# Kernel tuning notes

Measured on AMD Instinct MI355X. Metric: run time of the kernel, lower is better.

## Reference

```python
import jax, jax.numpy as jnp
import numpy as np

N = 50000
E = 800000
F_IN = 64
HID = 64
NCLS = 16


def setup_inputs() -> dict:
    key = jax.random.key(0)
    ks = jax.random.split(key, 8)
    x = jax.random.normal(ks[0], (N, F_IN), dtype=jnp.float32)
    edge_index = jax.random.randint(ks[1], (2, E), 0, N, dtype=jnp.int64)
    edge_weight = jax.random.uniform(ks[2], (E,), dtype=jnp.float32)
    # GCNConv glorot-style weights (PyG stores weight as [in, out]) and zero bias
    W1 = jax.random.normal(ks[3], (F_IN, HID), dtype=jnp.float32) * (1.0 / np.sqrt(F_IN))
    b1 = jnp.zeros((HID,), dtype=jnp.float32)
    W2 = jax.random.normal(ks[4], (HID, HID), dtype=jnp.float32) * (1.0 / np.sqrt(HID))
    b2 = jnp.zeros((HID,), dtype=jnp.float32)
    Wout = jax.random.normal(ks[5], (HID, NCLS), dtype=jnp.float32) * (1.0 / np.sqrt(HID))
    bout = jnp.zeros((NCLS,), dtype=jnp.float32)
    return {"x": x, "edge_index": edge_index, "edge_weight": edge_weight,
            "W1": W1, "b1": b1, "W2": W2, "b2": b2, "Wout": Wout, "bout": bout}


def _gcn_norm(edge_index, edge_weight, num_nodes):
    # PyG gcn_norm with add_self_loops=True (self-loop weight = 1.0)
    row = jnp.concatenate([edge_index[0], jnp.arange(num_nodes, dtype=edge_index.dtype)])
    col = jnp.concatenate([edge_index[1], jnp.arange(num_nodes, dtype=edge_index.dtype)])
    w = jnp.concatenate([edge_weight, jnp.ones((num_nodes,), dtype=edge_weight.dtype)])
    deg = jax.ops.segment_sum(w, col, num_segments=num_nodes)  # [N]
    dinv = jnp.where(deg > 0, jax.lax.rsqrt(deg), 0.0)
    norm = dinv[row] * w * dinv[col]  # [E+N]
    return row, col, norm


def _gcn_conv(h, row, col, norm, W, b, num_nodes):
    h = h @ W                                   # [N, out]
    msg = h[row] * norm[:, None]                # gather + scale, [E+N, out]
    out = jax.ops.segment_sum(msg, col, num_segments=num_nodes)  # scatter-add
    return out + b


def reference(x, edge_index, edge_weight, W1, b1, W2, b2, Wout, bout):
    num_nodes = x.shape[0]
    row, col, norm = _gcn_norm(edge_index, edge_weight, num_nodes)
    h = _gcn_conv(x, row, col, norm, W1, b1, num_nodes)
    h = jax.nn.relu(h)  # dropout is identity in eval mode
    h = _gcn_conv(h, row, col, norm, W2, b2, num_nodes)
    h = jax.nn.relu(h)
    logits = h @ Wout + bout
    return jax.nn.softmax(logits, axis=1)
```

## Files before the change

kernel.cpp:

```cpp
#include <hip/hip_runtime.h>
#include <hip/hip_fp16.h>
#include <math.h>

#define NN 50000
#define NE 800000
#define F 64
#define NCLS 16

#define BKS 7
#define BKN 128
#define NBK 391
#define CAP 2560
#define B1C 4096
#define B1B 196

typedef unsigned short u16;
typedef unsigned int u32;
typedef __attribute__((ext_vector_type(8))) unsigned short ushort8v;

__device__ __forceinline__ float bf2f(u16 h) {
    return __uint_as_float((unsigned)h << 16);
}
__device__ __forceinline__ u16 f2bf(float f) {
    unsigned u = __float_as_uint(f);
    return (u16)((u + 0x7fffu + ((u >> 16) & 1u)) >> 16);
}


__global__ __launch_bounds__(512) void k_local(const int* __restrict__ row,
                                               const int* __restrict__ col,
                                               const float* __restrict__ w,
                                               int2* __restrict__ tmp,
                                               int* __restrict__ ghL,
                                               int* __restrict__ ghH) {
    __shared__ int hist[512], sa[512], sb[512], lcur[512];
    __shared__ int2 stage[B1C];
    int t = threadIdx.x;
    int e0 = blockIdx.x * B1C;
    int cnt = min(B1C, NE - e0);
    hist[t] = 0;
    __syncthreads();

    int mykey[8]; int myb[8]; int myw[8]; bool myv[8];
#pragma unroll
    for (int k = 0; k < 8; ++k) {
        int i = t + k * 512;
        myv[k] = (i < cnt);
        if (myv[k]) {
            int e = e0 + i;
            int c = col[e];
            myb[k]   = c >> BKS;
            mykey[k] = (row[e] << BKS) | (c & (BKN - 1));
            myw[k]   = __float_as_int(w[e]);
            atomicAdd(&hist[myb[k]], 1);
        }
    }
    __syncthreads();

    sa[t] = hist[t];
    __syncthreads();
    int* src = sa; int* dst = sb;
#pragma unroll
    for (int off = 1; off < 512; off <<= 1) {
        dst[t] = src[t] + ((t >= off) ? src[t - off] : 0);
        __syncthreads();
        int* tq = src; src = dst; dst = tq;
    }
    int lex = src[t] - hist[t];
    lcur[t] = lex;
    ghL[blockIdx.x * 512 + t] = lex;
    ghH[blockIdx.x * 512 + t] = hist[t];
    __syncthreads();

#pragma unroll
    for (int k = 0; k < 8; ++k) {
        if (myv[k]) {
            int pos = atomicAdd(&lcur[myb[k]], 1);
            stage[pos] = make_int2(mykey[k], myw[k]);
        }
    }
    __syncthreads();

    for (int i = t; i < cnt; i += 512) tmp[e0 + i] = stage[i];
}


__global__ __launch_bounds__(256) void k_bucket2(const int2* __restrict__ tmp,
                                                 const int* __restrict__ ghL,
                                                 const int* __restrict__ ghH,
                                                 u32* __restrict__ sedge,
                                                 int2* __restrict__ benode,
                                                 float* __restrict__ dinv) {
    __shared__ int2 stage[CAP];
    __shared__ u32 sortedU[CAP];
    __shared__ int lb[200], ps[200];
    __shared__ int ssa[256], ssb[256];
    __shared__ int hist[BKN], na[BKN], nb[BKN], lcur[BKN];
    __shared__ float dsum[BKN];
    int b = blockIdx.x;
    int t = threadIdx.x;
    int lnv = 0;
    if (t < B1B) {
        lb[t] = ghL[t * 512 + b];
        lnv   = ghH[t * 512 + b];
    }
    if (t < BKN) { hist[t] = 0; dsum[t] = 0.f; }
    ssa[t] = lnv;
    __syncthreads();
    int* src = ssa; int* dst = ssb;
#pragma unroll
    for (int off = 1; off < 256; off <<= 1) {
        dst[t] = src[t] + ((t >= off) ? src[t - off] : 0);
        __syncthreads();
        int* tq = src; src = dst; dst = tq;
    }
    if (t < B1B) ps[t] = src[t] - lnv;
    __shared__ int cntS;
    if (t == 0) cntS = src[255];
    __syncthreads();
    int cnt = min(cntS, CAP);

    for (int i = t; i < cnt; i += 256) {
        int lo = 0, hi = B1B;
        while (hi - lo > 1) {
            int mid = (lo + hi) >> 1;
            if (ps[mid] <= i) lo = mid; else hi = mid;
        }
        int2 ed = tmp[lo * B1C + lb[lo] + (i - ps[lo])];
        stage[i] = ed;
        atomicAdd(&hist[ed.x & (BKN - 1)], 1);
        atomicAdd(&dsum[ed.x & (BKN - 1)], __int_as_float(ed.y));
    }
    __syncthreads();
    if (t < BKN) na[t] = hist[t];
    __syncthreads();
    int* s2 = na; int* d2 = nb;
#pragma unroll
    for (int off = 1; off < BKN; off <<= 1) {
        if (t < BKN) d2[t] = s2[t] + ((t >= off) ? s2[t - off] : 0);
        __syncthreads();
        int* tq = s2; s2 = d2; d2 = tq;
    }
    int node0 = b * BKN;
    if (t < BKN) {
        int lincl = s2[t];
        int lexcl = lincl - hist[t];
        lcur[t] = lexcl;
        int node = node0 + t;
        if (node < NN) {
            benode[node] = make_int2(b * CAP + lexcl, b * CAP + lincl);
            dinv[node]   = rsqrtf(1.0f + dsum[t]);
        }
    }
    __syncthreads();
    for (int i = t; i < cnt; i += 256) {
        int2 ed = stage[i];
        int pos = atomicAdd(&lcur[ed.x & (BKN - 1)], 1);
        __half hw = __float2half(__int_as_float(ed.y));
        u32 hb = (u32)__half_as_ushort(hw);
        sortedU[pos] = (hb << 16) | (u32)(ed.x >> BKS);
    }
    __syncthreads();
    for (int i = t; i < cnt; i += 256) sedge[b * CAP + i] = sortedU[i];
}


template<bool BF>
__global__ __launch_bounds__(256) void k_mm64(const void* __restrict__ Xv,
                                              const float* __restrict__ W,
                                              u16* __restrict__ Y) {
    __shared__ float sW[64 * 64];
    __shared__ float sX[16][64];
    int tid = threadIdx.x;
    int c  = tid & 63;
    int wv = tid >> 6;
    for (int i = tid; i < 64 * 64; i += 256) sW[i] = W[i];
    int r0 = blockIdx.x * 16;
#pragma unroll
    for (int i = tid; i < 16 * 64; i += 256) {
        size_t idx = (size_t)(r0 + (i >> 6)) * 64 + (i & 63);
        if (BF) sX[i >> 6][i & 63] = bf2f(((const u16*)Xv)[idx]);
        else    sX[i >> 6][i & 63] = ((const float*)Xv)[idx];
    }
    __syncthreads();
    int rb = wv * 4;
    float a0 = 0.f, a1 = 0.f, a2 = 0.f, a3 = 0.f;
#pragma unroll
    for (int k = 0; k < 64; k += 4) {
        float4 x0 = *(const float4*)&sX[rb + 0][k];
        float4 x1 = *(const float4*)&sX[rb + 1][k];
        float4 x2 = *(const float4*)&sX[rb + 2][k];
        float4 x3 = *(const float4*)&sX[rb + 3][k];
        float wA = sW[(k + 0) * 64 + c];
        float wB = sW[(k + 1) * 64 + c];
        float wC = sW[(k + 2) * 64 + c];
        float wD = sW[(k + 3) * 64 + c];
        a0 += x0.x * wA + x0.y * wB + x0.z * wC + x0.w * wD;
        a1 += x1.x * wA + x1.y * wB + x1.z * wC + x1.w * wD;
        a2 += x2.x * wA + x2.y * wB + x2.z * wC + x2.w * wD;
        a3 += x3.x * wA + x3.y * wB + x3.z * wC + x3.w * wD;
    }
    Y[(size_t)(r0 + rb + 0) * 64 + c] = f2bf(a0);
    Y[(size_t)(r0 + rb + 1) * 64 + c] = f2bf(a1);
    Y[(size_t)(r0 + rb + 2) * 64 + c] = f2bf(a2);
    Y[(size_t)(r0 + rb + 3) * 64 + c] = f2bf(a3);
}


template<bool HEAD>
__global__ __launch_bounds__(256) void k_agg(const u16* __restrict__ A,
                                             const int2* __restrict__ benode,
                                             const u32* __restrict__ sedge,
                                             const float* __restrict__ dinv,
                                             const float* __restrict__ bias,
                                             u16* __restrict__ B,
                                             const float* __restrict__ Wout,
                                             const float* __restrict__ bout,
                                             float* __restrict__ out) {
    __shared__ float sWout[64 * NCLS];
    __shared__ float sh[8][64];
    int tid  = threadIdx.x;
    int wv   = tid >> 6;
    int lane = tid & 63;
    int half = lane >> 5;
    int sub  = lane & 31;
    int slot = sub >> 3;
    int fg   = sub & 7;
    int node = blockIdx.x * 8 + wv * 2 + half;
    if (HEAD) {
        for (int i = tid; i < 64 * NCLS; i += 256) sWout[i] = Wout[i];
    }
    int2 be = benode[node];
    int beg = be.x;
    int deg = be.y - be.x;
    float acc[8] = {0.f, 0.f, 0.f, 0.f, 0.f, 0.f, 0.f, 0.f};

    {
        u32 e = (sub < deg) ? sedge[beg + sub] : 0u;
        int s_own = (int)(e & 0xffffu);
        float wf = __half2float(__ushort_as_half((u16)(e >> 16)));
        float nmr = wf * dinv[s_own];
        int mval = min(32, deg);
#pragma unroll
        for (int t = 0; t < 8; ++t) {
            if ((t << 2) < mval) {
                int idx = (half << 5) + (t << 2) + slot;
                int   s  = __shfl(s_own, idx);
                float nm = __shfl(nmr, idx);
                const ushort8v a = *(const ushort8v*)(A + (size_t)s * 64 + (fg << 3));
#pragma unroll
                for (int j = 0; j < 8; ++j) acc[j] += bf2f(a[j]) * nm;
            }
        }
    }
    for (int base = 32; base < deg; base += 32) {
        int i = base + sub;
        u32 e = (i < deg) ? sedge[beg + i] : 0u;
        int s_own = (int)(e & 0xffffu);
        float wf = __half2float(__ushort_as_half((u16)(e >> 16)));
        float nmr = wf * dinv[s_own];
        int m = min(32, deg - base);
        int steps = (m + 3) >> 2;
        for (int t = 0; t < steps; ++t) {
            int idx = (half << 5) + (t << 2) + slot;
            int   s  = __shfl(s_own, idx);
            float nm = __shfl(nmr, idx);
            const ushort8v a = *(const ushort8v*)(A + (size_t)s * 64 + (fg << 3));
#pragma unroll
            for (int j = 0; j < 8; ++j) acc[j] += bf2f(a[j]) * nm;
        }
    }
#pragma unroll
    for (int o = 8; o <= 16; o <<= 1) {
#pragma unroll
        for (int j = 0; j < 8; ++j) acc[j] += __shfl_xor(acc[j], o);
    }
    if (slot == 0) {
        float d = dinv[node];
        float d2 = d * d;
        const ushort8v self = *(const ushort8v*)(A + (size_t)node * 64 + (fg << 3));
        const float4 bb0 = *(const float4*)(bias + (fg << 3));
        const float4 bb1 = *(const float4*)(bias + (fg << 3) + 4);
        float bbv[8] = {bb0.x, bb0.y, bb0.z, bb0.w, bb1.x, bb1.y, bb1.z, bb1.w};
        ushort8v ov;
#pragma unroll
        for (int j = 0; j < 8; ++j) {
            float v = fmaxf(acc[j] * d + bf2f(self[j]) * d2 + bbv[j], 0.f);
            ov[j] = f2bf(v);
            if (HEAD) sh[wv * 2 + half][(fg << 3) + j] = v;
        }
        *(ushort8v*)(B + (size_t)node * 64 + (fg << 3)) = ov;
    }
    if (HEAD) {
        __syncthreads();
        int nib  = tid >> 5;
        int sub2 = tid & 31;
        int c = sub2 & 15, q = sub2 >> 4;
        const float* hrow = sh[nib];
        float p = 0.f;
#pragma unroll
        for (int k = 0; k < 32; ++k)
            p += hrow[q * 32 + k] * sWout[(q * 32 + k) * NCLS + c];
        p += __shfl_xor(p, 16);
        p += bout[c];
        float mx = p;
#pragma unroll
        for (int o = 8; o >= 1; o >>= 1) mx = fmaxf(mx, __shfl_xor(mx, o, 16));
        float ex = expf(p - mx);
        float s = ex;
#pragma unroll
        for (int o = 8; o >= 1; o >>= 1) s += __shfl_xor(s, o, 16);
        if (q == 0) out[(size_t)(blockIdx.x * 8 + nib) * NCLS + c] = ex / s;
    }
}


extern "C" void kernel_launch(void* const* d_in, const int* in_sizes, int n_in,
                              void* d_out, int out_size, void* d_ws, size_t ws_size,
                              hipStream_t stream) {
    const float* x    = (const float*)d_in[0];
    const int*   ei   = (const int*)d_in[1];
    const float* ew   = (const float*)d_in[2];
    const float* W1   = (const float*)d_in[3];
    const float* b1   = (const float*)d_in[4];
    const float* W2   = (const float*)d_in[5];
    const float* b2   = (const float*)d_in[6];
    const float* Wout = (const float*)d_in[7];
    const float* bout = (const float*)d_in[8];
    const int* row = ei;
    const int* col = ei + NE;

    int*   ip     = (int*)d_ws;
    int2*  benode = (int2*)ip;
    float* dinv   = (float*)(ip + 100096);
    int*   ghL    = ip + 150144;
    int*   ghH    = ghL + 100352;
    u32*   sedge  = (u32*)(ip + 350848);
    int2*  tmp    = (int2*)(ip + 350848 + NBK * CAP);
    u16*   A      = (u16*)(tmp + (size_t)B1B * B1C);
    u16*   B      = A + 3200000;

    k_mm64<false><<<NN / 16, 256, 0, stream>>>(x, W1, A);

    k_local<<<B1B, 512, 0, stream>>>(row, col, ew, tmp, ghL, ghH);
    k_bucket2<<<NBK, 256, 0, stream>>>(tmp, ghL, ghH, sedge, benode, dinv);

    k_agg<false><<<NN / 8, 256, 0, stream>>>(A, benode, sedge, dinv, b1, B,
                                             nullptr, nullptr, nullptr);
    k_mm64<true><<<NN / 16, 256, 0, stream>>>(B, W2, A);
    k_agg<true><<<NN / 8, 256, 0, stream>>>(A, benode, sedge, dinv, b2, B,
                                            Wout, bout, (float*)d_out);
}
```

Before: 189.0 us.

## Fuse layer-2 weight matmul into first aggregation epilogue

The first aggregation kernel now loads W2 into shared memory and, after computing the ReLU hidden row per node, multiplies it by W2 in-block and writes the transformed bf16 features directly. This removes the separate k_mm64 launch for layer 2 and the round trip through global memory of the intermediate hidden activations. The second aggregation becomes a dedicated head kernel with the softmax epilogue. The cost is that every aggregation block reloads the 16KB W2, and extra shared memory per block may reduce occupancy.

```diff
diff --git a/kernel.cpp b/kernel.cpp
--- a/kernel.cpp
+++ b/kernel.cpp
@@ -165,8 +165,7 @@
 }
 
 
-template<bool BF>
-__global__ __launch_bounds__(256) void k_mm64(const void* __restrict__ Xv,
+__global__ __launch_bounds__(256) void k_mm64(const float* __restrict__ X,
                                               const float* __restrict__ W,
                                               u16* __restrict__ Y) {
     __shared__ float sW[64 * 64];
@@ -177,11 +176,8 @@
     for (int i = tid; i < 64 * 64; i += 256) sW[i] = W[i];
     int r0 = blockIdx.x * 16;
 #pragma unroll
-    for (int i = tid; i < 16 * 64; i += 256) {
-        size_t idx = (size_t)(r0 + (i >> 6)) * 64 + (i & 63);
-        if (BF) sX[i >> 6][i & 63] = bf2f(((const u16*)Xv)[idx]);
-        else    sX[i >> 6][i & 63] = ((const float*)Xv)[idx];
-    }
+    for (int i = tid; i < 16 * 64; i += 256)
+        sX[i >> 6][i & 63] = X[(size_t)(r0 + (i >> 6)) * 64 + (i & 63)];
     __syncthreads();
     int rb = wv * 4;
     float a0 = 0.f, a1 = 0.f, a2 = 0.f, a3 = 0.f;
@@ -207,17 +203,14 @@
 }
 
 
-template<bool HEAD>
-__global__ __launch_bounds__(256) void k_agg(const u16* __restrict__ A,
-                                             const int2* __restrict__ benode,
-                                             const u32* __restrict__ sedge,
-                                             const float* __restrict__ dinv,
-                                             const float* __restrict__ bias,
-                                             u16* __restrict__ B,
-                                             const float* __restrict__ Wout,
-                                             const float* __restrict__ bout,
-                                             float* __restrict__ out) {
-    __shared__ float sWout[64 * NCLS];
+__global__ __launch_bounds__(256) void k_aggmm(const u16* __restrict__ A,
+                                               const int2* __restrict__ benode,
+                                               const u32* __restrict__ sedge,
+                                               const float* __restrict__ dinv,
+                                               const float* __restrict__ bias,
+                                               const float* __restrict__ W2,
+                                               u16* __restrict__ A2) {
+    __shared__ float sW2[64 * 64];
     __shared__ float sh[8][64];
     int tid  = threadIdx.x;
     int wv   = tid >> 6;
@@ -227,9 +220,8 @@
     int slot = sub >> 3;
     int fg   = sub & 7;
     int node = blockIdx.x * 8 + wv * 2 + half;
-    if (HEAD) {
-        for (int i = tid; i < 64 * NCLS; i += 256) sWout[i] = Wout[i];
-    }
+    for (int i = tid; i < 64 * 64; i += 256) sW2[i] = W2[i];
+
     int2 be = benode[node];
     int beg = be.x;
     int deg = be.y - be.x;
@@ -282,36 +274,125 @@
         const float4 bb0 = *(const float4*)(bias + (fg << 3));
         const float4 bb1 = *(const float4*)(bias + (fg << 3) + 4);
         float bbv[8] = {bb0.x, bb0.y, bb0.z, bb0.w, bb1.x, bb1.y, bb1.z, bb1.w};
-        ushort8v ov;
-#pragma unroll
-        for (int j = 0; j < 8; ++j) {
-            float v = fmaxf(acc[j] * d + bf2f(self[j]) * d2 + bbv[j], 0.f);
-            ov[j] = f2bf(v);
-            if (HEAD) sh[wv * 2 + half][(fg << 3) + j] = v;
-        }
-        *(ushort8v*)(B + (size_t)node * 64 + (fg << 3)) = ov;
-    }
-    if (HEAD) {
-        __syncthreads();
-        int nib  = tid >> 5;
-        int sub2 = tid & 31;
-        int c = sub2 & 15, q = sub2 >> 4;
-        const float* hrow = sh[nib];
-        float p = 0.f;
-#pragma unroll
-        for (int k = 0; k < 32; ++k)
-            p += hrow[q * 32 + k] * sWout[(q * 32 + k) * NCLS + c];
-        p += __shfl_xor(p, 16);
-        p += bout[c];
-        float mx = p;
-#pragma unroll
-        for (int o = 8; o >= 1; o >>= 1) mx = fmaxf(mx, __shfl_xor(mx, o, 16));
-        float ex = expf(p - mx);
-        float s = ex;
-#pragma unroll
-        for (int o = 8; o >= 1; o >>= 1) s += __shfl_xor(s, o, 16);
-        if (q == 0) out[(size_t)(blockIdx.x * 8 + nib) * NCLS + c] = ex / s;
-    }
+        int r = wv * 2 + half;
+#pragma unroll
+        for (int j = 0; j < 8; ++j)
+            sh[r][(fg << 3) + j] = fmaxf(acc[j] * d + bf2f(self[j]) * d2 + bbv[j], 0.f);
+    }
+    __syncthreads();
+
+    int nib = tid >> 5;
+    int c   = tid & 31;
+    const float* hrow = sh[nib];
+    float p0 = 0.f, p1 = 0.f;
+#pragma unroll
+    for (int k = 0; k < 64; k += 4) {
+        float4 hv = *(const float4*)&hrow[k];
+        p0 += hv.x * sW2[(k + 0) * 64 + c] + hv.y * sW2[(k + 1) * 64 + c]
+            + hv.z * sW2[(k + 2) * 64 + c] + hv.w * sW2[(k + 3) * 64 + c];
+        p1 += hv.x * sW2[(k + 0) * 64 + c + 32] + hv.y * sW2[(k + 1) * 64 + c + 32]
+            + hv.z * sW2[(k + 2) * 64 + c + 32] + hv.w * sW2[(k + 3) * 64 + c + 32];
+    }
+    int onode = blockIdx.x * 8 + nib;
+    A2[(size_t)onode * 64 + c]      = f2bf(p0);
+    A2[(size_t)onode * 64 + c + 32] = f2bf(p1);
+}
+
+
+__global__ __launch_bounds__(256) void k_agg2(const u16* __restrict__ A,
+                                              const int2* __restrict__ benode,
+                                              const u32* __restrict__ sedge,
+                                              const float* __restrict__ dinv,
+                                              const float* __restrict__ bias,
+                                              const float* __restrict__ Wout,
+                                              const float* __restrict__ bout,
+                                              float* __restrict__ out) {
+    __shared__ float sWout[64 * NCLS];
+    __shared__ float sh[8][64];
+    int tid  = threadIdx.x;
+    int wv   = tid >> 6;
+    int lane = tid & 63;
+    int half = lane >> 5;
+    int sub  = lane & 31;
+    int slot = sub >> 3;
+    int fg   = sub & 7;
+    int node = blockIdx.x * 8 + wv * 2 + half;
+    for (int i = tid; i < 64 * NCLS; i += 256) sWout[i] = Wout[i];
+    int2 be = benode[node];
+    int beg = be.x;
+    int deg = be.y - be.x;
+    float acc[8] = {0.f, 0.f, 0.f, 0.f, 0.f, 0.f, 0.f, 0.f};
+    {
+        u32 e = (sub < deg) ? sedge[beg + sub] : 0u;
+        int s_own = (int)(e & 0xffffu);
+        float wf = __half2float(__ushort_as_half((u16)(e >> 16)));
+        float nmr = wf * dinv[s_own];
+        int mval = min(32, deg);
+#pragma unroll
+        for (int t = 0; t < 8; ++t) {
+            if ((t << 2) < mval) {
+                int idx = (half << 5) + (t << 2) + slot;
+                int   s  = __shfl(s_own, idx);
+                float nm = __shfl(nmr, idx);
+                const ushort8v a = *(const ushort8v*)(A + (size_t)s * 64 + (fg << 3));
+#pragma unroll
+                for (int j = 0; j < 8; ++j) acc[j] += bf2f(a[j]) * nm;
+            }
+        }
+    }
+    for (int base = 32; base < deg; base += 32) {
+        int i = base + sub;
+        u32 e = (i < deg) ? sedge[beg + i] : 0u;
+        int s_own = (int)(e & 0xffffu);
+        float wf = __half2float(__ushort_as_half((u16)(e >> 16)));
+        float nmr = wf * dinv[s_own];
+        int m = min(32, deg - base);
+        int steps = (m + 3) >> 2;
+        for (int t = 0; t < steps; ++t) {
+            int idx = (half << 5) + (t << 2) + slot;
+            int   s  = __shfl(s_own, idx);
+            float nm = __shfl(nmr, idx);
+            const ushort8v a = *(const ushort8v*)(A + (size_t)s * 64 + (fg << 3));
+#pragma unroll
+            for (int j = 0; j < 8; ++j) acc[j] += bf2f(a[j]) * nm;
+        }
+    }
+#pragma unroll
+    for (int o = 8; o <= 16; o <<= 1) {
+#pragma unroll
+        for (int j = 0; j < 8; ++j) acc[j] += __shfl_xor(acc[j], o);
+    }
+    if (slot == 0) {
+        float d = dinv[node];
+        float d2 = d * d;
+        const ushort8v self = *(const ushort8v*)(A + (size_t)node * 64 + (fg << 3));
+        const float4 bb0 = *(const float4*)(bias + (fg << 3));
+        const float4 bb1 = *(const float4*)(bias + (fg << 3) + 4);
+        float bbv[8] = {bb0.x, bb0.y, bb0.z, bb0.w, bb1.x, bb1.y, bb1.z, bb1.w};
+        int r = wv * 2 + half;
+#pragma unroll
+        for (int j = 0; j < 8; ++j)
+            sh[r][(fg << 3) + j] = fmaxf(acc[j] * d + bf2f(self[j]) * d2 + bbv[j], 0.f);
+    }
+    __syncthreads();
+    int nib  = tid >> 5;
+    int sub2 = tid & 31;
+    int c = sub2 & 15, q = sub2 >> 4;
+    const float* hrow = sh[nib];
+    float p = 0.f;
+#pragma unroll
+    for (int k = 0; k < 32; ++k)
+        p += hrow[q * 32 + k] * sWout[(q * 32 + k) * NCLS + c];
+    p += __shfl_xor(p, 16);
+    p += bout[c];
+    float mx = p;
+#pragma unroll
+    for (int o = 8; o >= 1; o >>= 1) mx = fmaxf(mx, __shfl_xor(mx, o, 16));
+    float ex = expf(p - mx);
+    float s = ex;
+#pragma unroll
+    for (int o = 8; o >= 1; o >>= 1) s += __shfl_xor(s, o, 16);
+    if (q == 0) out[(size_t)(blockIdx.x * 8 + nib) * NCLS + c] = ex / s;
 }
 
 
@@ -340,14 +421,13 @@
     u16*   A      = (u16*)(tmp + (size_t)B1B * B1C);
     u16*   B      = A + 3200000;
 
-    k_mm64<false><<<NN / 16, 256, 0, stream>>>(x, W1, A);
+    k_mm64<<<NN / 16, 256, 0, stream>>>(x, W1, A);
 
     k_local<<<B1B, 512, 0, stream>>>(row, col, ew, tmp, ghL, ghH);
     k_bucket2<<<NBK, 256, 0, stream>>>(tmp, ghL, ghH, sedge, benode, dinv);
 
-    k_agg<false><<<NN / 8, 256, 0, stream>>>(A, benode, sedge, dinv, b1, B,
-                                             nullptr, nullptr, nullptr);
-    k_mm64<true><<<NN / 16, 256, 0, stream>>>(B, W2, A);
-    k_agg<true><<<NN / 8, 256, 0, stream>>>(A, benode, sedge, dinv, b2, B,
-                                            Wout, bout, (float*)d_out);
-}
+    k_aggmm<<<NN / 8, 256, 0, stream>>>(A, benode, sedge, dinv, b1, W2, B);
+
+    k_agg2<<<NN / 8, 256, 0, stream>>>(B, benode, sedge, dinv, b2,
+                                       Wout, bout, (float*)d_out);
+}
```

Result: faster. 183.1 us (-3.1%).
